# Kernel tuning notes

Hardware: AMD Instinct MI355X
Metric: run time of the kernel (lower is better)

Reference implementation:

```python
import jax, jax.numpy as jnp
import numpy as np

# Standard H36M 32-joint kinematic tree (parent of each joint; -1 = root/hip).
# parents[j] < j for all j, so joints can be processed in index order.
PARENTS = [-1, 0, 1, 2, 3, 4, 0, 6, 7, 8, 9, 0, 11, 12, 13, 14,
           12, 16, 17, 18, 19, 20, 19, 22, 12, 24, 25, 26, 27, 28, 27, 30]
NUM_JOINTS = 32
BATCH = 262144


def setup_inputs() -> dict:
    key = jax.random.key(0)
    k1, k2 = jax.random.split(key)
    angles = jax.random.normal(k1, (BATCH, NUM_JOINTS, 3, 3), dtype=jnp.float32)
    offsets = jax.random.normal(k2, (NUM_JOINTS, 3), dtype=jnp.float32)
    return {"angles": angles, "offsets": offsets}


def reference(angles, offsets):
    """Batched forward kinematics over the H36M 32-joint tree.

    angles:  [B, 32, 3, 3] local joint rotation matrices
    offsets: [32, 3]       bone offset (row) vectors
    returns: [B, 32, 3]    global joint positions (getJointPositions analogue)
    """
    B = angles.shape[0]
    pos = [None] * NUM_JOINTS
    rot = [None] * NUM_JOINTS
    # Root (hip): position zero, global rotation = local hip rotation.
    pos[0] = jnp.zeros((B, 3), dtype=angles.dtype)
    rot[0] = angles[:, 0]
    # Fixed-size loop over the kinematic chain (31 joints); batch dim vectorized.
    for j in range(1, NUM_JOINTS):
        p = PARENTS[j]
        # offset[j] (row vector) @ parent global rotation + parent position
        pos[j] = jnp.einsum('k,bkl->bl', offsets[j], rot[p]) + pos[p]
        # local rotation @ parent global rotation
        rot[j] = jnp.einsum('bik,bkl->bil', angles[:, j], rot[p])
    return jnp.stack(pos, axis=1)  # [B, 32, 3]
```

## Files before the change

### kernel.cpp

```cpp
#include <hip/hip_runtime.h>


__global__ __launch_bounds__(256) void fk32_kernel(
    const float* __restrict__ angles,
    const float* __restrict__ offsets,
    float* __restrict__ out,
    int B)
{
    const int b = blockIdx.x * 256 + threadIdx.x;
    if (b >= B) return;

    constexpr int PAR[32] = {-1,0,1,2,3,4,0,6,7,8,9,0,11,12,13,14,
                             12,16,17,18,19,20,19,22,12,24,25,26,27,28,27,30};

    const float4* __restrict__ ap = reinterpret_cast<const float4*>(angles) + (size_t)b * 72u;
    float4* __restrict__ op = reinterpret_cast<float4*>(out) + (size_t)b * 24u;

    float4 buf[2][9];
#pragma unroll
    for (int q = 0; q < 9; ++q) buf[0][q] = ap[q];

    float rot[32][3][3];
    float pos[32][3];

#pragma unroll
    for (int g = 0; g < 8; ++g) {
        if (g < 7) {
#pragma unroll
            for (int q = 0; q < 9; ++q) buf[(g + 1) & 1][q] = ap[(g + 1) * 9 + q];
        }

        float a[36];
#pragma unroll
        for (int q = 0; q < 9; ++q) {
            const float4 v = buf[g & 1][q];
            a[4*q+0] = v.x; a[4*q+1] = v.y; a[4*q+2] = v.z; a[4*q+3] = v.w;
        }

#pragma unroll
        for (int jj = 0; jj < 4; ++jj) {
            const int j = g * 4 + jj;
            if (j == 0) {
#pragma unroll
                for (int i = 0; i < 3; ++i)
#pragma unroll
                    for (int l = 0; l < 3; ++l)
                        rot[0][i][l] = a[i*3 + l];
                pos[0][0] = 0.f; pos[0][1] = 0.f; pos[0][2] = 0.f;
            } else {
                const int p = PAR[j];
                const float o0 = offsets[j*3+0];
                const float o1 = offsets[j*3+1];
                const float o2 = offsets[j*3+2];
#pragma unroll
                for (int l = 0; l < 3; ++l)
                    pos[j][l] = fmaf(o0, rot[p][0][l],
                               fmaf(o1, rot[p][1][l],
                               fmaf(o2, rot[p][2][l], pos[p][l])));
#pragma unroll
                for (int i = 0; i < 3; ++i) {
                    const float a0 = a[jj*9 + i*3 + 0];
                    const float a1 = a[jj*9 + i*3 + 1];
                    const float a2 = a[jj*9 + i*3 + 2];
#pragma unroll
                    for (int l = 0; l < 3; ++l)
                        rot[j][i][l] = fmaf(a0, rot[p][0][l],
                                      fmaf(a1, rot[p][1][l],
                                           a2 * rot[p][2][l]));
                }
            }
        }
    }

#pragma unroll
    for (int g = 0; g < 8; ++g) {
        op[g*3+0] = make_float4(pos[g*4+0][0], pos[g*4+0][1], pos[g*4+0][2], pos[g*4+1][0]);
        op[g*3+1] = make_float4(pos[g*4+1][1], pos[g*4+1][2], pos[g*4+2][0], pos[g*4+2][1]);
        op[g*3+2] = make_float4(pos[g*4+2][2], pos[g*4+3][0], pos[g*4+3][1], pos[g*4+3][2]);
    }
}

extern "C" void kernel_launch(void* const* d_in, const int* in_sizes, int n_in,
                              void* d_out, int out_size, void* d_ws, size_t ws_size,
                              hipStream_t stream) {
    const float* angles  = (const float*)d_in[0];
    const float* offsets = (const float*)d_in[1];
    float* out = (float*)d_out;
    const int B = in_sizes[0] / 288;
    const int block = 256;
    const int grid = (B + block - 1) / block;
    fk32_kernel<<<grid, block, 0, stream>>>(angles, offsets, out, B);
}
```

Baseline: 477.4 us.

## Stage angle loads through LDS with coalesced async global_load_lds double buffering

Replaces per-thread strided float4 loads of each batch element's rotation matrices with wave-cooperative loads, where consecutive lanes fetch consecutive 16-byte chunks. The loads go directly into shared memory via global_load_lds and are double-buffered across joint groups. Manual s_waitcnt vmcnt/lgkmcnt control the overlap. This aims to improve coalescing of the 1152-byte-per-element stride. The cost is extra LDS reads with a 9-float4 stride per lane, which may cause bank conflicts. The bounds check was also dropped, so B must be a multiple of 256.

```diff
diff --git a/kernel.cpp b/kernel.cpp
--- a/kernel.cpp
+++ b/kernel.cpp
@@ -1,5 +1,9 @@
 #include <hip/hip_runtime.h>
 
+
+#define ASM_VMCNT9() asm volatile("s_waitcnt vmcnt(9)" ::: "memory")
+#define ASM_VMCNT0() asm volatile("s_waitcnt vmcnt(0)" ::: "memory")
+#define ASM_LGKM0()  asm volatile("s_waitcnt lgkmcnt(0)" ::: "memory")
 
 __global__ __launch_bounds__(256) void fk32_kernel(
     const float* __restrict__ angles,
@@ -7,18 +11,34 @@
     float* __restrict__ out,
     int B)
 {
-    const int b = blockIdx.x * 256 + threadIdx.x;
-    if (b >= B) return;
-
     constexpr int PAR[32] = {-1,0,1,2,3,4,0,6,7,8,9,0,11,12,13,14,
                              12,16,17,18,19,20,19,22,12,24,25,26,27,28,27,30};
 
-    const float4* __restrict__ ap = reinterpret_cast<const float4*>(angles) + (size_t)b * 72u;
-    float4* __restrict__ op = reinterpret_cast<float4*>(out) + (size_t)b * 24u;
+    const int wid   = threadIdx.x >> 6;
+    const int lane  = threadIdx.x & 63;
+    const int wbase = blockIdx.x * 256 + wid * 64;
+    const int b     = wbase + lane;
 
-    float4 buf[2][9];
+    __shared__ float4 lds[2][4][576];
+
+    const float4* __restrict__ gbase =
+        reinterpret_cast<const float4*>(angles) + (size_t)wbase * 72u;
+
+    const float4* gp[9];
 #pragma unroll
-    for (int q = 0; q < 9; ++q) buf[0][q] = ap[q];
+    for (int t = 0; t < 9; ++t) {
+        const int n = t * 64 + lane;
+        const int e = n / 9;
+        const int q = n - e * 9;
+        gp[t] = gbase + (e * 72 + q);
+    }
+
+#pragma unroll
+    for (int t = 0; t < 9; ++t)
+        __builtin_amdgcn_global_load_lds(
+            (const __attribute__((address_space(1))) void*)(gp[t]),
+            (__attribute__((address_space(3))) void*)(&lds[0][wid][t * 64]),
+            16, 0, 0);
 
     float rot[32][3][3];
     float pos[32][3];
@@ -26,14 +46,20 @@
 #pragma unroll
     for (int g = 0; g < 8; ++g) {
         if (g < 7) {
+            ASM_LGKM0();
 #pragma unroll
-            for (int q = 0; q < 9; ++q) buf[(g + 1) & 1][q] = ap[(g + 1) * 9 + q];
+            for (int t = 0; t < 9; ++t)
+                __builtin_amdgcn_global_load_lds(
+                    (const __attribute__((address_space(1))) void*)(gp[t] + 9 * (g + 1)),
+                    (__attribute__((address_space(3))) void*)(&lds[(g + 1) & 1][wid][t * 64]),
+                    16, 0, 0);
         }
+        if (g == 7) { ASM_VMCNT0(); } else { ASM_VMCNT9(); }
 
         float a[36];
 #pragma unroll
         for (int q = 0; q < 9; ++q) {
-            const float4 v = buf[g & 1][q];
+            const float4 v = lds[g & 1][wid][lane * 9 + q];
             a[4*q+0] = v.x; a[4*q+1] = v.y; a[4*q+2] = v.z; a[4*q+3] = v.w;
         }
 
@@ -72,6 +98,7 @@
         }
     }
 
+    float4* __restrict__ op = reinterpret_cast<float4*>(out) + (size_t)b * 24u;
 #pragma unroll
     for (int g = 0; g < 8; ++g) {
         op[g*3+0] = make_float4(pos[g*4+0][0], pos[g*4+0][1], pos[g*4+0][2], pos[g*4+1][0]);
```

Result: faster. 444.9 us (-6.8%).
